# Optimization experiments

Measured on AMD Instinct MI355X. Metric: run time of the kernel, lower is better.

Reference implementation:

```python
import jax, jax.numpy as jnp
import numpy as np

N_EMBD = 1024
N_HEAD = 16
HEAD = N_EMBD // N_HEAD


def setup_inputs() -> dict:
    key = jax.random.key(0)
    ks = jax.random.split(key, 6)
    B, S = 4, 2048
    scale = 1.0 / np.sqrt(N_EMBD)
    return {
        "x": jax.random.normal(ks[0], (B, S, N_EMBD), dtype=jnp.float32),
        "Wq": jax.random.normal(ks[1], (N_EMBD, N_EMBD), dtype=jnp.float32) * scale,
        "Wk": jax.random.normal(ks[2], (N_EMBD, N_EMBD), dtype=jnp.float32) * scale,
        "Wv": jax.random.normal(ks[3], (N_EMBD, N_EMBD), dtype=jnp.float32) * scale,
        "Wo": jax.random.normal(ks[4], (N_EMBD, N_EMBD), dtype=jnp.float32) * scale,
        "bo": jnp.zeros((N_EMBD,), dtype=jnp.float32),
    }


def reference(x, Wq, Wk, Wv, Wo, bo):
    B, S, _ = x.shape
    # projections; nn.Linear applies x @ W.T but W is random here, so x @ W is equivalent math
    def split_heads(t):  # (B,S,E) -> (B,H,S,D)
        return t.reshape(B, S, N_HEAD, HEAD).transpose(0, 2, 1, 3)

    q = split_heads(x @ Wq)
    k = split_heads(x @ Wk)
    v = split_heads(x @ Wv)
    scores = jnp.einsum("bhqd,bhkd->bhqk", q, k) * (HEAD ** -0.5)
    causal = jnp.tril(jnp.ones((S, S), dtype=bool))
    scores = jnp.where(causal, scores, -jnp.inf)
    weights = jax.nn.softmax(scores, axis=-1)  # dropout p=0 (eval)
    out = jnp.einsum("bhqk,bhkd->bhqd", weights, v)
    out = out.transpose(0, 2, 1, 3).reshape(B, S, N_EMBD)
    return out @ Wo + bo
```

## Files before the change

kernel.cpp:

```cpp
#include <hip/hip_runtime.h>
#include <hip/hip_bf16.h>

typedef unsigned short u16;
typedef unsigned int u32;
typedef __bf16 bf16x8 __attribute__((ext_vector_type(8)));
typedef float f32x4 __attribute__((ext_vector_type(4)));
typedef u16 u16x8 __attribute__((ext_vector_type(8)));
typedef u16 u16x4 __attribute__((ext_vector_type(4)));

#define NB 4
#define SEQ 2048
#define EMB 1024
#define NHEAD 16
#define DHEAD 64
#define MTOT (NB*SEQ)

static __device__ __forceinline__ u16 f2bf(float f) {
  union { __bf16 h; u16 u; } cv;
  cv.h = (__bf16)f;
  return cv.u;
}

static __device__ __forceinline__ float fexp2(float x) {
  float r;
  asm("v_exp_f32 %0, %1" : "=v"(r) : "v"(x));
  return r;
}

static __device__ __forceinline__ void gload16(const void* g, void* l) {
  __builtin_amdgcn_global_load_lds((const __attribute__((address_space(1))) void*)g,
                                   (__attribute__((address_space(3))) void*)l, 16, 0, 0);
}


__global__ __launch_bounds__(256) void k_cvt_x(const float* __restrict__ in, u16* __restrict__ out) {
  size_t i = (size_t)blockIdx.x * 256 + threadIdx.x;
  const float4* p = (const float4*)in + i * 2;
  float4 a = p[0], b = p[1];
  u16x8 r;
  r[0] = f2bf(a.x); r[1] = f2bf(a.y); r[2] = f2bf(a.z); r[3] = f2bf(a.w);
  r[4] = f2bf(b.x); r[5] = f2bf(b.y); r[6] = f2bf(b.z); r[7] = f2bf(b.w);
  *(u16x8*)(out + i * 8) = r;
}

__global__ __launch_bounds__(256) void k_wtrans(const float* __restrict__ W0, const float* __restrict__ W1,
                                                const float* __restrict__ W2, const float* __restrict__ W3,
                                                u16* __restrict__ O0, u16* __restrict__ O1,
                                                u16* __restrict__ O2, u16* __restrict__ O3) {
  __shared__ float tile[64][65];
  const float* W = blockIdx.z == 0 ? W0 : blockIdx.z == 1 ? W1 : blockIdx.z == 2 ? W2 : W3;
  u16* O       = blockIdx.z == 0 ? O0 : blockIdx.z == 1 ? O1 : blockIdx.z == 2 ? O2 : O3;
  const int c0 = blockIdx.x * 64, r0 = blockIdx.y * 64;
  const int t = threadIdx.x;
  const int tr = t >> 4, tc = (t & 15) * 4;
#pragma unroll
  for (int p = 0; p < 4; p++) {
    int r = tr + p * 16;
    float4 v = *(const float4*)&W[(size_t)(r0 + r) * EMB + c0 + tc];
    tile[r][tc + 0] = v.x; tile[r][tc + 1] = v.y; tile[r][tc + 2] = v.z; tile[r][tc + 3] = v.w;
  }
  __syncthreads();
#pragma unroll
  for (int p = 0; p < 4; p++) {
    int orow = tr + p * 16;
    u16x4 o;
    o[0] = f2bf(tile[tc + 0][orow]); o[1] = f2bf(tile[tc + 1][orow]);
    o[2] = f2bf(tile[tc + 2][orow]); o[3] = f2bf(tile[tc + 3][orow]);
    *(u16x4*)&O[(size_t)(c0 + orow) * EMB + r0 + tc] = o;
  }
}


static __device__ __forceinline__ void gemm_core(const u16* __restrict__ A, const u16* __restrict__ BT,
                                                 int m0, int n0, f32x4 acc[4][4]) {
  __shared__ u16 As[2][128 * 64];
  __shared__ u16 Bs[2][128 * 64];
  const int t = threadIdx.x, l = t & 63, w = t >> 6;
  const int g = l >> 4, q = l & 15;
  const int wm = (w >> 1) * 64, wn = (w & 1) * 64;

  const f32x4 zero4 = {0.f, 0.f, 0.f, 0.f};
#pragma unroll
  for (int mi = 0; mi < 4; mi++)
#pragma unroll
    for (int ni = 0; ni < 4; ni++) acc[mi][ni] = zero4;

  int srow[4], skel[4];
#pragma unroll
  for (int i = 0; i < 4; i++) {
    int row = w * 32 + i * 8 + (l >> 3);
    srow[i] = row; skel[i] = ((l & 7) ^ (row & 7)) * 8;
  }

  auto stage = [&](int k0, int bsel) {
    char* AsB = (char*)As[bsel] + w * 4096;
    char* BsB = (char*)Bs[bsel] + w * 4096;
#pragma unroll
    for (int i = 0; i < 4; i++) {
      gload16(A + (size_t)(m0 + srow[i]) * EMB + k0 + skel[i], AsB + i * 1024);
      gload16(BT + (size_t)(n0 + srow[i]) * EMB + k0 + skel[i], BsB + i * 1024);
    }
  };

  auto compute = [&](int bsel) {
    char* AsB = (char*)As[bsel];
    char* BsB = (char*)Bs[bsel];
#pragma unroll
    for (int kc = 0; kc < 2; kc++) {
      bf16x8 af[4], bfv[4];
#pragma unroll
      for (int mi = 0; mi < 4; mi++) {
        int row = wm + mi * 16 + q;
        af[mi] = *(const bf16x8*)(AsB + row * 128 + (((kc * 4 + g) ^ (row & 7)) << 4));
      }
#pragma unroll
      for (int ni = 0; ni < 4; ni++) {
        int row = wn + ni * 16 + q;
        bfv[ni] = *(const bf16x8*)(BsB + row * 128 + (((kc * 4 + g) ^ (row & 7)) << 4));
      }
      __builtin_amdgcn_s_setprio(1);
#pragma unroll
      for (int mi = 0; mi < 4; mi++)
#pragma unroll
        for (int ni = 0; ni < 4; ni++)
          acc[mi][ni] = __builtin_amdgcn_mfma_f32_16x16x32_bf16(af[mi], bfv[ni], acc[mi][ni], 0, 0, 0);
      __builtin_amdgcn_s_setprio(0);
    }
  };

  stage(0, 0);
  int buf = 0;
  for (int k0 = 64; k0 <= EMB; k0 += 64) {
    const bool pf = (k0 < EMB);
    if (pf) {
      stage(k0, buf ^ 1);
      asm volatile("s_waitcnt vmcnt(8)" ::: "memory");
    } else {
      asm volatile("s_waitcnt vmcnt(0)" ::: "memory");
    }
    __builtin_amdgcn_s_barrier();
    __builtin_amdgcn_sched_barrier(0);
    compute(buf);
    asm volatile("s_waitcnt lgkmcnt(0)" ::: "memory");
    __builtin_amdgcn_s_barrier();
    buf ^= 1;
  }
}

__global__ __launch_bounds__(512, 2) void k_gemm_qkv(const u16* __restrict__ xb, const u16* __restrict__ Wqkv,
                                                     u16* __restrict__ Qb, u16* __restrict__ Kb, u16* __restrict__ Vb) {
  __shared__ u16 As[2][256 * 64];
  __shared__ u16 Bs[2][256 * 64];
  const int t = threadIdx.x, l = t & 63, wid = t >> 6;
  const int g = l >> 4, q = l & 15;
  const int wr = wid >> 2, wc = wid & 3;

  const int wg = blockIdx.x;
  const int c = wg & 7, local = wg >> 3;
  const int idx = c * 48 + local;
  const int ni_ = idx >> 5, mi_ = idx & 31;
  const int m0 = mi_ * 256, n0 = ni_ * 256;

  f32x4 acc[2][2][4][2];
  const f32x4 zero4 = {0.f, 0.f, 0.f, 0.f};
#pragma unroll
  for (int R = 0; R < 2; R++)
#pragma unroll
    for (int C = 0; C < 2; C++)
#pragma unroll
      for (int mi = 0; mi < 4; mi++)
#pragma unroll
        for (int ni = 0; ni < 2; ni++) acc[R][C][mi][ni] = zero4;

  int srow[2], skel[2];
#pragma unroll
  for (int j = 0; j < 2; j++) {
    int row = j * 64 + (t >> 3);
    srow[j] = row; skel[j] = ((t & 7) ^ (row & 7)) * 8;
  }

  auto stageHalf = [&](int op, int half, int tile) {
    if (tile >= 16) return;
    const int kk = tile * 64, d = tile & 1;
    const u16* src = op ? Wqkv : xb;
    const int base = op ? n0 : m0;
    char* dst = (char*)(op ? Bs[d] : As[d]) + half * 16384 + wid * 1024;
#pragma unroll
    for (int j = 0; j < 2; j++)
      gload16(src + (size_t)(base + half * 128 + srow[j]) * EMB + kk + skel[j], dst + j * 8192);
  };

  bf16x8 af[4][2], bf0[2][2], bf1[2][2];
  auto loadA = [&](int R, int d) {
    char* Ab = (char*)As[d];
#pragma unroll
    for (int mi = 0; mi < 4; mi++)
#pragma unroll
      for (int kc = 0; kc < 2; kc++) {
        int row = R * 128 + wr * 64 + mi * 16 + q;
        af[mi][kc] = *(const bf16x8*)(Ab + row * 128 + (((kc * 4 + g) ^ (row & 7)) << 4));
      }
  };
  auto loadB = [&](int C, int d, bf16x8 (&bfv)[2][2]) {
    char* Bb = (char*)Bs[d];
#pragma unroll
    for (int ni = 0; ni < 2; ni++)
#pragma unroll
      for (int kc = 0; kc < 2; kc++) {
        int row = C * 128 + wc * 32 + ni * 16 + q;
        bfv[ni][kc] = *(const bf16x8*)(Bb + row * 128 + (((kc * 4 + g) ^ (row & 7)) << 4));
      }
  };

#define MFMA16(R, C, BF)                                                                   \
  do {                                                                                     \
    __builtin_amdgcn_s_setprio(1);                                                         \
    _Pragma("unroll")                                                                      \
    for (int kc = 0; kc < 2; kc++)                                                         \
      _Pragma("unroll")                                                                    \
      for (int mi = 0; mi < 4; mi++)                                                       \
        _Pragma("unroll")                                                                  \
        for (int ni = 0; ni < 2; ni++)                                                     \
          acc[R][C][mi][ni] = __builtin_amdgcn_mfma_f32_16x16x32_bf16(af[mi][kc], BF[ni][kc], acc[R][C][mi][ni], 0, 0, 0); \
    __builtin_amdgcn_s_setprio(0);                                                         \
  } while (0)

  stageHalf(0, 0, 0); stageHalf(1, 0, 0); stageHalf(1, 1, 0); stageHalf(0, 1, 0);
  stageHalf(0, 0, 1); stageHalf(1, 1, 1);
  asm volatile("s_waitcnt vmcnt(4)" ::: "memory");
  __builtin_amdgcn_s_barrier();
  __builtin_amdgcn_sched_barrier(0);

  for (int kt = 0; kt < 16; ++kt) {
    const int d = kt & 1;
    loadA(0, d); loadB(0, d, bf0);
    stageHalf(0, 1, kt + 1);
    __builtin_amdgcn_s_barrier();
    MFMA16(0, 0, bf0);
    __builtin_amdgcn_s_barrier();
    __builtin_amdgcn_sched_barrier(0);
    loadB(1, d, bf1);
    stageHalf(1, 0, kt + 1);
    __builtin_amdgcn_s_barrier();
    MFMA16(0, 1, bf1);
    __builtin_amdgcn_s_barrier();
    __builtin_amdgcn_sched_barrier(0);
    loadA(1, d);
    stageHalf(0, 0, kt + 2);
    __builtin_amdgcn_s_barrier();
    MFMA16(1, 1, bf1);
    __builtin_amdgcn_s_barrier();
    __builtin_amdgcn_sched_barrier(0);
    stageHalf(1, 1, kt + 2);
    __builtin_amdgcn_s_barrier();
    MFMA16(1, 0, bf0);
    if (kt <= 13)      asm volatile("s_waitcnt vmcnt(4)" ::: "memory");
    else if (kt == 14) asm volatile("s_waitcnt vmcnt(0)" ::: "memory");
    __builtin_amdgcn_s_barrier();
    __builtin_amdgcn_sched_barrier(0);
  }
#undef MFMA16

  const int z = n0 >> 10;
  u16* Out = z == 0 ? Qb : (z == 1 ? Kb : Vb);
  const float scale = z == 0 ? 0.125f * 1.4426950408889634f : 1.0f;

#pragma unroll
  for (int R = 0; R < 2; R++)
#pragma unroll
    for (int C = 0; C < 2; C++)
#pragma unroll
      for (int mi = 0; mi < 4; mi++)
#pragma unroll
        for (int ni = 0; ni < 2; ni++)
#pragma unroll
          for (int jj = 0; jj < 4; jj++) {
            int m = m0 + R * 128 + wr * 64 + mi * 16 + g * 4 + jj;
            int n = n0 + C * 128 + wc * 32 + ni * 16 + q;
            int b = m >> 11, s = m & 2047;
            int col = n & 1023;
            int h = col >> 6, dd = col & 63;
            Out[(((size_t)(b * NHEAD + h)) * SEQ + s) * DHEAD + dd] = f2bf(acc[R][C][mi][ni][jj] * scale);
          }
}

__global__ __launch_bounds__(256) void k_gemm_out(const u16* __restrict__ Ob, const u16* __restrict__ WoT,
                                                  const float* __restrict__ bo, float* __restrict__ out) {
  const int wg = blockIdx.x;
  const int c = wg & 7, local = wg >> 3;
  const int m0 = (local & 63) * 128, n0 = c * 128;

  f32x4 acc[4][4];
  gemm_core(Ob, WoT, m0, n0, acc);

  const int t = threadIdx.x, l = t & 63, w = t >> 6;
  const int g = l >> 4, q = l & 15;
  const int wm = (w >> 1) * 64, wn = (w & 1) * 64;
#pragma unroll
  for (int ni = 0; ni < 4; ni++) {
    int n = n0 + wn + ni * 16 + q;
    float bv = bo[n];
#pragma unroll
    for (int mi = 0; mi < 4; mi++)
#pragma unroll
      for (int jj = 0; jj < 4; jj++) {
        int m = m0 + wm + mi * 16 + g * 4 + jj;
        out[(size_t)m * EMB + n] = acc[mi][ni][jj] + bv;
      }
  }
}

__global__ __launch_bounds__(256, 4) void k_attn(const u16* __restrict__ Qb, const u16* __restrict__ Kb,
                                                 const u16* __restrict__ Vb, u16* __restrict__ Ob) {
  __shared__ u16 Ks[2][64 * 64];
  __shared__ u16 Vt[2][64 * 64];
  const int t = threadIdx.x, l = t & 63, w = t >> 6;
  const int g = l >> 4, q = l & 15;
  const int bh = blockIdx.x;
  const int b = bh >> 4, h = bh & 15;
  const size_t hb = (size_t)bh * SEQ * DHEAD;
  const float NEG_INF = -__builtin_inff();

  const int i = blockIdx.y;
  const int qA0 = i * 64, qB0 = (31 - i) * 64;
  const int ntA = i + 1, ntB = 32 - i;

  int krow[2], kel[2];
#pragma unroll
  for (int ii = 0; ii < 2; ii++) {
    int row = w * 16 + ii * 8 + (l >> 3);
    krow[ii] = row; kel[ii] = ((l & 7) ^ (row & 7)) * 8;
  }
  const int kp = t & 31, d0v = (t >> 5) * 8;
  const int r2 = 2 * kp;
  const int sp = 32 * ((r2 >> 4) >> 1) + 8 * ((r2 >> 2) & 3) + 4 * ((r2 >> 4) & 1) + (r2 & 3);

  int olds[2][4], owv[8];
#pragma unroll
  for (int kc = 0; kc < 2; kc++)
#pragma unroll
    for (int kf = 0; kf < 4; kf++) {
      int row = kf * 16 + q;
      olds[kc][kf] = row * 128 + (((kc * 4 + g) ^ (row & 7)) << 4);
    }
#pragma unroll
  for (int ii = 0; ii < 8; ii++) {
    int d = d0v + ii;
    owv[ii] = d * 128 + ((sp * 2) ^ ((d & 7) << 4));
  }

  const u16* kgp0 = Kb + hb + (size_t)krow[0] * DHEAD + kel[0];
  const u16* kgp1 = Kb + hb + (size_t)krow[1] * DHEAD + kel[1];
  const u16* vgp0 = Vb + hb + (size_t)(2 * kp) * DHEAD + d0v;
  const u16* vgp1 = vgp0 + DHEAD;

  auto stageK = [&](const u16* p0, const u16* p1, int bsel) {
    char* dst = (char*)Ks[bsel] + w * 2048;
    gload16(p0, dst);
    gload16(p1, dst + 1024);
  };
  auto writeV = [&](int bsel, const u16x8& v0, const u16x8& v1) {
    char* VtB = (char*)Vt[bsel];
#pragma unroll
    for (int ii = 0; ii < 8; ii++) {
      u32 val = (u32)v0[ii] | ((u32)v1[ii] << 16);
      *(u32*)(VtB + owv[ii]) = val;
    }
  };

  bf16x8 qfA[2], qfB[2];
#pragma unroll
  for (int kc = 0; kc < 2; kc++) {
    qfA[kc] = *(const bf16x8*)(Qb + hb + (size_t)(qA0 + w * 16 + q) * DHEAD + kc * 32 + g * 8);
    qfB[kc] = *(const bf16x8*)(Qb + hb + (size_t)(qB0 + w * 16 + q) * DHEAD + kc * 32 + g * 8);
  }
  const int qglobA = qA0 + w * 16 + q, qglobB = qB0 + w * 16 + q;

  f32x4 oA[4], oB[4];
  const f32x4 zero4 = {0.f, 0.f, 0.f, 0.f};
#pragma unroll
  for (int df = 0; df < 4; df++) { oA[df] = zero4; oB[df] = zero4; }
  float mA = NEG_INF, lA = 0.f, mB = NEG_INF, lB = 0.f;

  auto compute = [&](const bf16x8 (&qf)[2], f32x4 (&o)[4], float& m_run, float& l_run,
                     bool diag, int qglob, int k0, const char* KsB, const char* VtB) {
    f32x4 st[4];
#pragma unroll
    for (int kf = 0; kf < 4; kf++) st[kf] = zero4;
    __builtin_amdgcn_s_setprio(1);
#pragma unroll
    for (int kc = 0; kc < 2; kc++)
#pragma unroll
      for (int kf = 0; kf < 4; kf++) {
        bf16x8 a = *(const bf16x8*)(KsB + olds[kc][kf]);
        st[kf] = __builtin_amdgcn_mfma_f32_16x16x32_bf16(a, qf[kc], st[kf], 0, 0, 0);
      }
    __builtin_amdgcn_s_setprio(0);

    if (diag) {
#pragma unroll
      for (int kf = 0; kf < 4; kf++)
#pragma unroll
        for (int jj = 0; jj < 4; jj++)
          if (k0 + kf * 16 + g * 4 + jj > qglob) st[kf][jj] = NEG_INF;
    }

    float x0 = fmaxf(fmaxf(st[0][0], st[0][1]), st[0][2]);
    float x1 = fmaxf(fmaxf(st[0][3], st[1][0]), st[1][1]);
    float x2 = fmaxf(fmaxf(st[1][2], st[1][3]), st[2][0]);
    float x3 = fmaxf(fmaxf(st[2][1], st[2][2]), st[2][3]);
    float x4 = fmaxf(fmaxf(st[3][0], st[3][1]), st[3][2]);
    float smax = fmaxf(fmaxf(x0, x1), x2);
    smax = fmaxf(fmaxf(smax, x3), x4);
    smax = fmaxf(smax, st[3][3]);
    smax = fmaxf(smax, __shfl_xor(smax, 16));
    smax = fmaxf(smax, __shfl_xor(smax, 32));

    if (!__all(smax - m_run <= 8.0f)) {
      float mnew = fmaxf(m_run, smax);
      float sc = fexp2(m_run - mnew);
      l_run *= sc;
#pragma unroll
      for (int jj = 0; jj < 4; jj++) {
        float scj = __shfl(sc, g * 4 + jj);
#pragma unroll
        for (int df = 0; df < 4; df++) o[df][jj] *= scj;
      }
      m_run = mnew;
    }

    f32x4 pv[4];
#pragma unroll
    for (int kf = 0; kf < 4; kf++)
#pragma unroll
      for (int jj = 0; jj < 4; jj++)
        pv[kf][jj] = fexp2(st[kf][jj] - m_run);
    f32x4 sv = (pv[0] + pv[1]) + (pv[2] + pv[3]);
    l_run += (sv[0] + sv[1]) + (sv[2] + sv[3]);

    bf16x8 pa[2];
    pa[0] = bf16x8{ (__bf16)pv[0][0], (__bf16)pv[0][1], (__bf16)pv[0][2], (__bf16)pv[0][3],
                    (__bf16)pv[1][0], (__bf16)pv[1][1], (__bf16)pv[1][2], (__bf16)pv[1][3] };
    pa[1] = bf16x8{ (__bf16)pv[2][0], (__bf16)pv[2][1], (__bf16)pv[2][2], (__bf16)pv[2][3],
                    (__bf16)pv[3][0], (__bf16)pv[3][1], (__bf16)pv[3][2], (__bf16)pv[3][3] };

    __builtin_amdgcn_s_setprio(1);
#pragma unroll
    for (int kc = 0; kc < 2; kc++)
#pragma unroll
      for (int df = 0; df < 4; df++) {
        bf16x8 vb = *(const bf16x8*)(VtB + olds[kc][df]);
        o[df] = __builtin_amdgcn_mfma_f32_16x16x32_bf16(pa[kc], vb, o[df], 0, 0, 0);
      }
    __builtin_amdgcn_s_setprio(0);
  };

  {
    u16x8 v0 = *(const u16x8*)vgp0, v1 = *(const u16x8*)vgp1;
    stageK(kgp0, kgp1, 0);
    writeV(0, v0, v1);
    kgp0 += 4096; kgp1 += 4096; vgp0 += 4096; vgp1 += 4096;
  }
  __syncthreads();

  int buf = 0;
  for (int kt = 0; kt < ntB; ++kt) {
    const int k0 = kt * 64;
    const bool pf = (kt + 1 < ntB);
    u16x8 nv0, nv1;
    if (pf) {
      stageK(kgp0, kgp1, buf ^ 1);
      nv0 = *(const u16x8*)vgp0; nv1 = *(const u16x8*)vgp1;
      kgp0 += 4096; kgp1 += 4096; vgp0 += 4096; vgp1 += 4096;
    }
    const char* KsB = (const char*)Ks[buf];
    const char* VtB = (const char*)Vt[buf];

    compute(qfB, oB, mB, lB, kt == ntB - 1, qglobB, k0, KsB, VtB);
    if (kt < ntA)
      compute(qfA, oA, mA, lA, kt == ntA - 1, qglobA, k0, KsB, VtB);

    if (pf) writeV(buf ^ 1, nv0, nv1);
    __syncthreads();
    buf ^= 1;
  }

  lA += __shfl_xor(lA, 16); lA += __shfl_xor(lA, 32);
  lB += __shfl_xor(lB, 16); lB += __shfl_xor(lB, 32);

  auto store = [&](f32x4 (&o)[4], float l_run, int q0) {
    float inv = 1.f / l_run;
#pragma unroll
    for (int jj = 0; jj < 4; jj++) {
      float r = __shfl(inv, g * 4 + jj);
      int s = q0 + w * 16 + g * 4 + jj;
#pragma unroll
      for (int df = 0; df < 4; df++)
        Ob[((size_t)(b * SEQ + s)) * EMB + h * DHEAD + df * 16 + q] = f2bf(o[df][jj] * r);
    }
  };
  store(oA, lA, qA0);
  store(oB, lB, qB0);
}


extern "C" void kernel_launch(void* const* d_in, const int* in_sizes, int n_in,
                              void* d_out, int out_size, void* d_ws, size_t ws_size,
                              hipStream_t stream) {
  const float* x  = (const float*)d_in[0];
  const float* Wq = (const float*)d_in[1];
  const float* Wk = (const float*)d_in[2];
  const float* Wv = (const float*)d_in[3];
  const float* Wo = (const float*)d_in[4];
  const float* bo = (const float*)d_in[5];
  float* out = (float*)d_out;

  char* ws = (char*)d_ws;
  u16* xb  = (u16*)(ws);
  u16* WqT = (u16*)(ws + (16u << 20));
  u16* WkT = WqT + (size_t)EMB * EMB;
  u16* WvT = WkT + (size_t)EMB * EMB;
  u16* WoT = WvT + (size_t)EMB * EMB;
  u16* Qb  = (u16*)(ws + (24u << 20));
  u16* Kb  = Qb + (size_t)MTOT * EMB;
  u16* Vb  = Kb + (size_t)MTOT * EMB;
  u16* Ob  = Vb + (size_t)MTOT * EMB;

  k_cvt_x<<<dim3(4096), 256, 0, stream>>>(x, xb);
  k_wtrans<<<dim3(16, 16, 4), 256, 0, stream>>>(Wq, Wk, Wv, Wo, WqT, WkT, WvT, WoT);
  k_gemm_qkv<<<dim3(384), 512, 0, stream>>>(xb, WqT, Qb, Kb, Vb);
  k_attn<<<dim3(64, 16), 256, 0, stream>>>(Qb, Kb, Vb, Ob);
  k_gemm_out<<<dim3(512), 256, 0, stream>>>(Ob, WoT, bo, out);
}
```

Measured before the change: 165.9 us.

## Split paired causal attention blocks into one query tile per block with heavy-first ordering

Replaces the load-balanced scheme, where each block handled two mirrored query tiles that shared K/V loads, with one 64-row query tile per block across 2048 blocks. Blocks are ordered longest-first, and the bh index is interleaved in groups of 8 so that neighbouring blocks likely land on different XCDs and work is spread. Launch bounds rise to 8 blocks per CU because each block now keeps half the register state. The cost is that each K/V tile is loaded and staged twice as often across the grid, since shared K/V reuse between the paired tiles is lost.

```diff
diff --git a/kernel.cpp b/kernel.cpp
--- a/kernel.cpp
+++ b/kernel.cpp
@@ -310,20 +310,23 @@
   }
 }
 
-__global__ __launch_bounds__(256, 4) void k_attn(const u16* __restrict__ Qb, const u16* __restrict__ Kb,
+__global__ __launch_bounds__(256, 8) void k_attn(const u16* __restrict__ Qb, const u16* __restrict__ Kb,
                                                  const u16* __restrict__ Vb, u16* __restrict__ Ob) {
   __shared__ u16 Ks[2][64 * 64];
   __shared__ u16 Vt[2][64 * 64];
   const int t = threadIdx.x, l = t & 63, w = t >> 6;
   const int g = l >> 4, q = l & 15;
-  const int bh = blockIdx.x;
+
+  const int bid = blockIdx.x;
+  const int c = bid & 7, loc = bid >> 3;
+  const int bh = c + 8 * (loc >> 5);
+  const int qt = 31 - (loc & 31);
   const int b = bh >> 4, h = bh & 15;
   const size_t hb = (size_t)bh * SEQ * DHEAD;
   const float NEG_INF = -__builtin_inff();
 
-  const int i = blockIdx.y;
-  const int qA0 = i * 64, qB0 = (31 - i) * 64;
-  const int ntA = i + 1, ntB = 32 - i;
+  const int q0 = qt * 64;
+  const int ntile = qt + 1;
 
   int krow[2], kel[2];
 #pragma unroll
@@ -368,22 +371,39 @@
     }
   };
 
-  bf16x8 qfA[2], qfB[2];
-#pragma unroll
-  for (int kc = 0; kc < 2; kc++) {
-    qfA[kc] = *(const bf16x8*)(Qb + hb + (size_t)(qA0 + w * 16 + q) * DHEAD + kc * 32 + g * 8);
-    qfB[kc] = *(const bf16x8*)(Qb + hb + (size_t)(qB0 + w * 16 + q) * DHEAD + kc * 32 + g * 8);
-  }
-  const int qglobA = qA0 + w * 16 + q, qglobB = qB0 + w * 16 + q;
-
-  f32x4 oA[4], oB[4];
+  bf16x8 qf[2];
+#pragma unroll
+  for (int kc = 0; kc < 2; kc++)
+    qf[kc] = *(const bf16x8*)(Qb + hb + (size_t)(q0 + w * 16 + q) * DHEAD + kc * 32 + g * 8);
+  const int qglob = q0 + w * 16 + q;
+
+  f32x4 o[4];
   const f32x4 zero4 = {0.f, 0.f, 0.f, 0.f};
 #pragma unroll
-  for (int df = 0; df < 4; df++) { oA[df] = zero4; oB[df] = zero4; }
-  float mA = NEG_INF, lA = 0.f, mB = NEG_INF, lB = 0.f;
-
-  auto compute = [&](const bf16x8 (&qf)[2], f32x4 (&o)[4], float& m_run, float& l_run,
-                     bool diag, int qglob, int k0, const char* KsB, const char* VtB) {
+  for (int df = 0; df < 4; df++) o[df] = zero4;
+  float m_run = NEG_INF, l_run = 0.f;
+
+  {
+    u16x8 v0 = *(const u16x8*)vgp0, v1 = *(const u16x8*)vgp1;
+    stageK(kgp0, kgp1, 0);
+    writeV(0, v0, v1);
+    kgp0 += 4096; kgp1 += 4096; vgp0 += 4096; vgp1 += 4096;
+  }
+  __syncthreads();
+
+  int buf = 0;
+  for (int kt = 0; kt < ntile; ++kt) {
+    const int k0 = kt * 64;
+    const bool pf = (kt + 1 < ntile);
+    u16x8 nv0, nv1;
+    if (pf) {
+      stageK(kgp0, kgp1, buf ^ 1);
+      nv0 = *(const u16x8*)vgp0; nv1 = *(const u16x8*)vgp1;
+      kgp0 += 4096; kgp1 += 4096; vgp0 += 4096; vgp1 += 4096;
+    }
+    const char* KsB = (const char*)Ks[buf];
+    const char* VtB = (const char*)Vt[buf];
+
     f32x4 st[4];
 #pragma unroll
     for (int kf = 0; kf < 4; kf++) st[kf] = zero4;
@@ -397,7 +417,7 @@
       }
     __builtin_amdgcn_s_setprio(0);
 
-    if (diag) {
+    if (kt == ntile - 1) {
 #pragma unroll
       for (int kf = 0; kf < 4; kf++)
 #pragma unroll
@@ -453,54 +473,23 @@
         o[df] = __builtin_amdgcn_mfma_f32_16x16x32_bf16(pa[kc], vb, o[df], 0, 0, 0);
       }
     __builtin_amdgcn_s_setprio(0);
-  };
-
-  {
-    u16x8 v0 = *(const u16x8*)vgp0, v1 = *(const u16x8*)vgp1;
-    stageK(kgp0, kgp1, 0);
-    writeV(0, v0, v1);
-    kgp0 += 4096; kgp1 += 4096; vgp0 += 4096; vgp1 += 4096;
-  }
-  __syncthreads();
-
-  int buf = 0;
-  for (int kt = 0; kt < ntB; ++kt) {
-    const int k0 = kt * 64;
-    const bool pf = (kt + 1 < ntB);
-    u16x8 nv0, nv1;
-    if (pf) {
-      stageK(kgp0, kgp1, buf ^ 1);
-      nv0 = *(const u16x8*)vgp0; nv1 = *(const u16x8*)vgp1;
-      kgp0 += 4096; kgp1 += 4096; vgp0 += 4096; vgp1 += 4096;
-    }
-    const char* KsB = (const char*)Ks[buf];
-    const char* VtB = (const char*)Vt[buf];
-
-    compute(qfB, oB, mB, lB, kt == ntB - 1, qglobB, k0, KsB, VtB);
-    if (kt < ntA)
-      compute(qfA, oA, mA, lA, kt == ntA - 1, qglobA, k0, KsB, VtB);
 
     if (pf) writeV(buf ^ 1, nv0, nv1);
     __syncthreads();
     buf ^= 1;
   }
 
-  lA += __shfl_xor(lA, 16); lA += __shfl_xor(lA, 32);
-  lB += __shfl_xor(lB, 16); lB += __shfl_xor(lB, 32);
-
-  auto store = [&](f32x4 (&o)[4], float l_run, int q0) {
-    float inv = 1.f / l_run;
-#pragma unroll
-    for (int jj = 0; jj < 4; jj++) {
-      float r = __shfl(inv, g * 4 + jj);
-      int s = q0 + w * 16 + g * 4 + jj;
-#pragma unroll
-      for (int df = 0; df < 4; df++)
-        Ob[((size_t)(b * SEQ + s)) * EMB + h * DHEAD + df * 16 + q] = f2bf(o[df][jj] * r);
-    }
-  };
-  store(oA, lA, qA0);
-  store(oB, lB, qB0);
+  l_run += __shfl_xor(l_run, 16);
+  l_run += __shfl_xor(l_run, 32);
+  float inv = 1.f / l_run;
+#pragma unroll
+  for (int jj = 0; jj < 4; jj++) {
+    float r = __shfl(inv, g * 4 + jj);
+    int s = q0 + w * 16 + g * 4 + jj;
+#pragma unroll
+    for (int df = 0; df < 4; df++)
+      Ob[((size_t)(b * SEQ + s)) * EMB + h * DHEAD + df * 16 + q] = f2bf(o[df][jj] * r);
+  }
 }
 
 
@@ -529,6 +518,6 @@
   k_cvt_x<<<dim3(4096), 256, 0, stream>>>(x, xb);
   k_wtrans<<<dim3(16, 16, 4), 256, 0, stream>>>(Wq, Wk, Wv, Wo, WqT, WkT, WvT, WoT);
   k_gemm_qkv<<<dim3(384), 512, 0, stream>>>(xb, WqT, Qb, Kb, Vb);
-  k_attn<<<dim3(64, 16), 256, 0, stream>>>(Qb, Kb, Vb, Ob);
+  k_attn<<<dim3(2048), 256, 0, stream>>>(Qb, Kb, Vb, Ob);
   k_gemm_out<<<dim3(512), 256, 0, stream>>>(Ob, WoT, bo, out);
 }
```

New measurement: 189.7 us. 1.14x slower.

## Halve QKV GEMM K-tile to 32 and raise occupancy to four blocks per CU

Applied to the files above, without the earlier changes.

The QKV projection GEMM now stages 32-wide K tiles instead of 64-wide ones. This halves LDS use per block and fragment registers per wave, and launch bounds now ask for 4 blocks per CU so more waves can hide latency. The swizzle is rewritten for 64-byte rows, and the loop runs 32 iterations with adjusted vmcnt waits. The cost is twice as many barriers and loop iterations per unit of work, and it is unclear whether the register budget allows 4 blocks with the 64 accumulator vectors still held per thread.

```diff
diff --git a/kernel.cpp b/kernel.cpp
--- a/kernel.cpp
+++ b/kernel.cpp
@@ -147,10 +147,10 @@
   }
 }
 
-__global__ __launch_bounds__(512, 2) void k_gemm_qkv(const u16* __restrict__ xb, const u16* __restrict__ Wqkv,
+__global__ __launch_bounds__(512, 4) void k_gemm_qkv(const u16* __restrict__ xb, const u16* __restrict__ Wqkv,
                                                      u16* __restrict__ Qb, u16* __restrict__ Kb, u16* __restrict__ Vb) {
-  __shared__ u16 As[2][256 * 64];
-  __shared__ u16 Bs[2][256 * 64];
+  __shared__ u16 As[2][256 * 32];
+  __shared__ u16 Bs[2][256 * 32];
   const int t = threadIdx.x, l = t & 63, wid = t >> 6;
   const int g = l >> 4, q = l & 15;
   const int wr = wid >> 2, wc = wid & 3;
@@ -172,94 +172,82 @@
 #pragma unroll
         for (int ni = 0; ni < 2; ni++) acc[R][C][mi][ni] = zero4;
 
-  int srow[2], skel[2];
-#pragma unroll
-  for (int j = 0; j < 2; j++) {
-    int row = j * 64 + (t >> 3);
-    srow[j] = row; skel[j] = ((t & 7) ^ (row & 7)) * 8;
-  }
+  const int srow = t >> 2;
+  const int skel = (((t & 3) + (srow >> 1)) & 3) * 8;
 
   auto stageHalf = [&](int op, int half, int tile) {
-    if (tile >= 16) return;
-    const int kk = tile * 64, d = tile & 1;
+    if (tile >= 32) return;
+    const int kk = tile * 32, d = tile & 1;
     const u16* src = op ? Wqkv : xb;
     const int base = op ? n0 : m0;
-    char* dst = (char*)(op ? Bs[d] : As[d]) + half * 16384 + wid * 1024;
-#pragma unroll
-    for (int j = 0; j < 2; j++)
-      gload16(src + (size_t)(base + half * 128 + srow[j]) * EMB + kk + skel[j], dst + j * 8192);
-  };
-
-  bf16x8 af[4][2], bf0[2][2], bf1[2][2];
+    char* dst = (char*)(op ? Bs[d] : As[d]) + half * 8192 + wid * 1024;
+    gload16(src + (size_t)(base + half * 128 + srow) * EMB + kk + skel, dst);
+  };
+
+  bf16x8 af[4], bf0[2], bf1[2];
   auto loadA = [&](int R, int d) {
-    char* Ab = (char*)As[d];
-#pragma unroll
-    for (int mi = 0; mi < 4; mi++)
-#pragma unroll
-      for (int kc = 0; kc < 2; kc++) {
-        int row = R * 128 + wr * 64 + mi * 16 + q;
-        af[mi][kc] = *(const bf16x8*)(Ab + row * 128 + (((kc * 4 + g) ^ (row & 7)) << 4));
-      }
-  };
-  auto loadB = [&](int C, int d, bf16x8 (&bfv)[2][2]) {
-    char* Bb = (char*)Bs[d];
-#pragma unroll
-    for (int ni = 0; ni < 2; ni++)
-#pragma unroll
-      for (int kc = 0; kc < 2; kc++) {
-        int row = C * 128 + wc * 32 + ni * 16 + q;
-        bfv[ni][kc] = *(const bf16x8*)(Bb + row * 128 + (((kc * 4 + g) ^ (row & 7)) << 4));
-      }
-  };
-
-#define MFMA16(R, C, BF)                                                                   \
+    char* Ab = (char*)As[d] + R * 8192;
+#pragma unroll
+    for (int mi = 0; mi < 4; mi++) {
+      int w_ = wr * 64 + mi * 16 + q;
+      af[mi] = *(const bf16x8*)(Ab + w_ * 64 + (((g - (w_ >> 1)) & 3) << 4));
+    }
+  };
+  auto loadB = [&](int C, int d, bf16x8 (&bfv)[2]) {
+    char* Bb = (char*)Bs[d] + C * 8192;
+#pragma unroll
+    for (int ni = 0; ni < 2; ni++) {
+      int w_ = wc * 32 + ni * 16 + q;
+      bfv[ni] = *(const bf16x8*)(Bb + w_ * 64 + (((g - (w_ >> 1)) & 3) << 4));
+    }
+  };
+
+#define MFMA8(R, C, BF)                                                                    \
   do {                                                                                     \
     __builtin_amdgcn_s_setprio(1);                                                         \
     _Pragma("unroll")                                                                      \
-    for (int kc = 0; kc < 2; kc++)                                                         \
+    for (int mi = 0; mi < 4; mi++)                                                         \
       _Pragma("unroll")                                                                    \
-      for (int mi = 0; mi < 4; mi++)                                                       \
-        _Pragma("unroll")                                                                  \
-        for (int ni = 0; ni < 2; ni++)                                                     \
-          acc[R][C][mi][ni] = __builtin_amdgcn_mfma_f32_16x16x32_bf16(af[mi][kc], BF[ni][kc], acc[R][C][mi][ni], 0, 0, 0); \
+      for (int ni = 0; ni < 2; ni++)                                                       \
+        acc[R][C][mi][ni] = __builtin_amdgcn_mfma_f32_16x16x32_bf16(af[mi], BF[ni], acc[R][C][mi][ni], 0, 0, 0); \
     __builtin_amdgcn_s_setprio(0);                                                         \
   } while (0)
 
   stageHalf(0, 0, 0); stageHalf(1, 0, 0); stageHalf(1, 1, 0); stageHalf(0, 1, 0);
   stageHalf(0, 0, 1); stageHalf(1, 1, 1);
-  asm volatile("s_waitcnt vmcnt(4)" ::: "memory");
+  asm volatile("s_waitcnt vmcnt(2)" ::: "memory");
   __builtin_amdgcn_s_barrier();
   __builtin_amdgcn_sched_barrier(0);
 
-  for (int kt = 0; kt < 16; ++kt) {
+  for (int kt = 0; kt < 32; ++kt) {
     const int d = kt & 1;
     loadA(0, d); loadB(0, d, bf0);
     stageHalf(0, 1, kt + 1);
     __builtin_amdgcn_s_barrier();
-    MFMA16(0, 0, bf0);
+    MFMA8(0, 0, bf0);
     __builtin_amdgcn_s_barrier();
     __builtin_amdgcn_sched_barrier(0);
     loadB(1, d, bf1);
     stageHalf(1, 0, kt + 1);
     __builtin_amdgcn_s_barrier();
-    MFMA16(0, 1, bf1);
+    MFMA8(0, 1, bf1);
     __builtin_amdgcn_s_barrier();
     __builtin_amdgcn_sched_barrier(0);
     loadA(1, d);
     stageHalf(0, 0, kt + 2);
     __builtin_amdgcn_s_barrier();
-    MFMA16(1, 1, bf1);
+    MFMA8(1, 1, bf1);
     __builtin_amdgcn_s_barrier();
     __builtin_amdgcn_sched_barrier(0);
     stageHalf(1, 1, kt + 2);
     __builtin_amdgcn_s_barrier();
-    MFMA16(1, 0, bf0);
-    if (kt <= 13)      asm volatile("s_waitcnt vmcnt(4)" ::: "memory");
-    else if (kt == 14) asm volatile("s_waitcnt vmcnt(0)" ::: "memory");
+    MFMA8(1, 0, bf0);
+    if (kt <= 29)      asm volatile("s_waitcnt vmcnt(2)" ::: "memory");
+    else if (kt == 30) asm volatile("s_waitcnt vmcnt(0)" ::: "memory");
     __builtin_amdgcn_s_barrier();
     __builtin_amdgcn_sched_barrier(0);
   }
-#undef MFMA16
+#undef MFMA8
 
   const int z = n0 >> 10;
   u16* Out = z == 0 ? Qb : (z == 1 ? Kb : Vb);
```

New measurement: 562.7 us. 3.39x slower.
